# Optimization experiments

Measured on AMD Instinct MI355X. Metric: run time of the kernel, lower is better.

## Reference

```python
import jax, jax.numpy as jnp
import numpy as np

K = 12
ORDERS = [(1, 2, 3), (1, 3, 2), (3, 2, 1), (3, 1, 2), (2, 1, 3), (2, 3, 1)]


def ranking_3d(x):
    # x: (B, L1, W1, H1, D) -> (B, 12, L1*W1*H1, D)
    B, L1, W1, H1, D = x.shape
    seqs = []
    for dims in ORDERS:
        perm = (0,) + dims + (4,)
        seqs.append(jnp.transpose(x, perm).reshape(B, -1, D))
        xr = jnp.flip(x, axis=dims)
        seqs.append(jnp.transpose(xr, perm).reshape(B, -1, D))
    return jnp.stack(seqs, axis=1)


def restore_original(out_y, shape):
    # out_y: (B, 12, D, L). NOTE: faithfully replicates the original code, which
    # reshapes the (B, D, L) slice directly to (B, d1, d2, d3, D).
    B, L1, W1, H1, D = shape
    size = {1: L1, 2: W1, 3: H1}
    restored = []
    for i in range(12):
        dims = ORDERS[i // 2]
        seq = out_y[:, i]  # (B, D, L)
        dims_shape = tuple(size[d] for d in dims)
        reshaped = seq.reshape((B,) + dims_shape + (D,))
        perm = (0,) + dims + (4,)
        inv = tuple(np.argsort(perm))
        r = jnp.transpose(reshaped, inv)
        if i % 2 == 1:
            r = jnp.flip(r, axis=dims)
        restored.append(r)
    return restored


def selective_scan(u, delta, A, Bs, Cs):
    # u, delta: (B,K,D,L); A: (K,D,N); Bs, Cs: (B,K,N,L)
    us = jnp.moveaxis(u, -1, 0)       # (L,B,K,D)
    ds = jnp.moveaxis(delta, -1, 0)   # (L,B,K,D)
    Bts = jnp.moveaxis(Bs, -1, 0)     # (L,B,K,N)
    Cts = jnp.moveaxis(Cs, -1, 0)     # (L,B,K,N)
    h0 = jnp.zeros(u.shape[:-1] + (A.shape[-1],), u.dtype)  # (B,K,D,N)

    def step(h, inp):
        ut, dt, Bt, Ct = inp
        dA = jnp.exp(dt[..., None] * A)                       # (B,K,D,N)
        h = dA * h + (dt * ut)[..., None] * Bt[:, :, None, :]
        y = jnp.einsum('bkdn,bkn->bkd', h, Ct)
        return h, y

    _, ys = jax.lax.scan(step, h0, (us, ds, Bts, Cts))
    return jnp.moveaxis(ys, 0, -1)  # (B,K,D,L)


def setup_inputs() -> dict:
    key = jax.random.key(0)
    ks = jax.random.split(key, 8)
    B, H, W, Len, D = 1, 16, 16, 16, 128
    N, R = 16, 8
    x = jax.random.normal(ks[0], (B, H, W, Len, D), dtype=jnp.float32)
    x_proj_weight = jax.random.normal(ks[1], (K, R + 2 * N, D), dtype=jnp.float32) * 0.02
    std = R ** -0.5
    dt_projs_weight = jax.random.uniform(ks[2], (K, D, R), minval=-std, maxval=std, dtype=jnp.float32)
    dt = jnp.exp(jax.random.uniform(ks[3], (K, D)) * (np.log(0.1) - np.log(0.001)) + np.log(0.001))
    dt = jnp.clip(dt, 1e-4, None)
    dt_projs_bias = (dt + jnp.log(-jnp.expm1(-dt))).astype(jnp.float32)
    A_logs = jnp.broadcast_to(jnp.log(jnp.arange(1, N + 1, dtype=jnp.float32)), (K, D, N)).copy()
    Ds = jnp.ones((K, D), dtype=jnp.float32)
    merge_w = jax.random.normal(ks[4], (K,), dtype=jnp.float32) * (1.0 / K)
    merge_b = jax.random.normal(ks[5], (), dtype=jnp.float32) * 0.01
    return {'x': x, 'x_proj_weight': x_proj_weight, 'dt_projs_weight': dt_projs_weight,
            'dt_projs_bias': dt_projs_bias, 'A_logs': A_logs, 'Ds': Ds,
            'merge_w': merge_w, 'merge_b': merge_b}


def reference(x, x_proj_weight, dt_projs_weight, dt_projs_bias, A_logs, Ds, merge_w, merge_b):
    B, H, W, Len, D = x.shape
    L = H * W * Len
    R = dt_projs_weight.shape[-1]
    N = A_logs.shape[-1]
    xs = jnp.transpose(ranking_3d(x), (0, 1, 3, 2))  # (B,K,D,L)
    x_dbl = jnp.einsum('bkdl,kcd->bkcl', xs, x_proj_weight)  # (B,K,R+2N,L)
    dts, Bs, Cs = jnp.split(x_dbl, [R, R + N], axis=2)
    dts = jnp.einsum('bkrl,kdr->bkdl', dts, dt_projs_weight)
    delta = jax.nn.softplus(dts + dt_projs_bias[None, :, :, None])
    A = -jnp.exp(A_logs)  # (K,D,N)
    ys = selective_scan(xs, delta, A, Bs, Cs)
    out_y = ys + Ds[None, :, :, None] * xs  # (B,K,D,L)
    restored = restore_original(out_y, (B, H, W, Len, D))
    stacked = jnp.stack(restored, axis=1)  # (B,K,H,W,Len,D)
    # mergeconv: 1x1 Conv2d over K channels == weighted sum across directions
    y = jnp.einsum('bkhwld,k->bhwld', stacked, merge_w) + merge_b
    return y
```

## Files before the change

### kernel.cpp

```cpp
#include <hip/hip_runtime.h>

#define KK 12
#define LL 4096
#define DD 128
#define NN 16
#define RR 8
#define NC 128
#define LC 32
#define XST 132
#define SDST 44
#define XDBL_TILE (LC * SDST)

__device__ __forceinline__ int pos_of(int k, int l) {
    int o = k >> 1;
    int le = (k & 1) ? (4095 - l) : l;
    int t1 = le >> 8, t2 = (le >> 4) & 15, t3 = le & 15;
    switch (o) {
        case 0:  return (t1 << 8) | (t2 << 4) | t3;
        case 1:  return (t1 << 8) | (t3 << 4) | t2;
        case 2:  return (t3 << 8) | (t2 << 4) | t1;
        case 3:  return (t2 << 8) | (t3 << 4) | t1;
        case 4:  return (t2 << 8) | (t1 << 4) | t3;
        default: return (t3 << 8) | (t1 << 4) | t2;
    }
}

__device__ __forceinline__ float delta_row_z(const float* sdbl, int l,
                                             float4 w0, float4 w1, float bz) {
    const float4* dr = (const float4*)(sdbl + l * SDST);
    float4 r0 = dr[0], r1 = dr[1];
    return bz + w0.x * r0.x + w0.y * r0.y + w0.z * r0.z + w0.w * r0.w
              + w1.x * r1.x + w1.y * r1.y + w1.z * r1.z + w1.w * r1.w;
}

__device__ __forceinline__ bool load_A8(const float* __restrict__ A_logs,
                                        int k, int d, int n0, float* A8, float& A0) {
    const float4* ap = (const float4*)(A_logs + ((size_t)(k * DD + d) * NN + n0));
    float4 a0 = ap[0], a1 = ap[1];
    A8[0] = -__expf(a0.x); A8[1] = -__expf(a0.y);
    A8[2] = -__expf(a0.z); A8[3] = -__expf(a0.w);
    A8[4] = -__expf(a1.x); A8[5] = -__expf(a1.y);
    A8[6] = -__expf(a1.z); A8[7] = -__expf(a1.w);
    A0 = -__expf(A_logs[(size_t)(k * DD + d) * NN]);
    bool s = (fabsf(A0 + 1.0f) <= 1e-5f);
    #pragma unroll
    for (int j = 0; j < 8; j++) {
        float m = (float)(n0 + j + 1);
        s = s && (fabsf(A8[j] - m * A0) <= 1e-4f * m * fabsf(A0));
    }
    return s;
}

template<bool S>
__device__ __forceinline__ void scan_step(
    float* xs, const float* sdbl, int i, int d, int half, int n0,
    const float* A8, float dt, float q, float Dval, float* h, float& dsum)
{
    float u = xs[i * XST + d];
    dsum += dt;
    float tu = dt * u;
    float e[8];
    if constexpr (S) {
        float q2 = q * q, q4 = q2 * q2, q8 = q4 * q4;
        e[0] = half ? q8 * q : q;
        #pragma unroll
        for (int j = 1; j < 8; j++) e[j] = e[j - 1] * q;
    } else {
        #pragma unroll
        for (int j = 0; j < 8; j++) e[j] = __expf(dt * A8[j]);
    }
    const float4* bp = (const float4*)(&sdbl[i * SDST + 8 + n0]);
    float4 b0 = bp[0], b1 = bp[1];
    const float4* cp = (const float4*)(&sdbl[i * SDST + 24 + n0]);
    float4 c0 = cp[0], c1 = cp[1];
    h[0] = e[0] * h[0] + tu * b0.x;  h[1] = e[1] * h[1] + tu * b0.y;
    h[2] = e[2] * h[2] + tu * b0.z;  h[3] = e[3] * h[3] + tu * b0.w;
    h[4] = e[4] * h[4] + tu * b1.x;  h[5] = e[5] * h[5] + tu * b1.y;
    h[6] = e[6] * h[6] + tu * b1.z;  h[7] = e[7] * h[7] + tu * b1.w;
    float yp = h[0] * c0.x + h[1] * c0.y + h[2] * c0.z + h[3] * c0.w
             + h[4] * c1.x + h[5] * c1.y + h[6] * c1.z + h[7] * c1.w;
    float yv = yp + __shfl_xor(yp, 1) + Dval * u;
    if (!half) xs[i * XST + d] = yv;
}

template<bool S>
__device__ __forceinline__ void scanA_body(
    float* xs, const float* sdbl, int k, int c,
    int d, int half, int n0, const float* A8,
    float4 w0, float4 w1, float bz, float Dval,
    float* __restrict__ S_g, float* __restrict__ dtsum)
{
    float h[8] = {0, 0, 0, 0, 0, 0, 0, 0};
    float dsum = 0.0f;

    #pragma unroll 2
    for (int i2 = 0; i2 < LC; i2 += 2) {
        float z = delta_row_z(sdbl, i2 + half, w0, w1, bz);
        float E = __expf(-fabsf(z));
        float opE = 1.0f + E;
        float dt = fmaxf(z, 0.0f) + __logf(opE);
        float q = 0.0f;
        if constexpr (S)
            q = (z >= 0.0f ? E : 1.0f) * __builtin_amdgcn_rcpf(opE);
        float dto = __shfl_xor(dt, 1);
        float qo  = S ? __shfl_xor(q, 1) : 0.0f;
        float dt0 = half ? dto : dt,  dt1 = half ? dt : dto;
        float q0  = half ? qo  : q,   q1  = half ? q  : qo;
        scan_step<S>(xs, sdbl, i2,     d, half, n0, A8, dt0, q0, Dval, h, dsum);
        scan_step<S>(xs, sdbl, i2 + 1, d, half, n0, A8, dt1, q1, Dval, h, dsum);
    }

    float4* sp = (float4*)(S_g + (((size_t)(k * NC + c) * DD + d) * NN + n0));
    sp[0] = make_float4(h[0], h[1], h[2], h[3]);
    sp[1] = make_float4(h[4], h[5], h[6], h[7]);
    if (!half) dtsum[(k * NC + c) * DD + d] = dsum;
}

__global__ __launch_bounds__(256, 4) void k1_proj_scanA(
    const float* __restrict__ x, const float* __restrict__ Wp,
    const float* __restrict__ Wdt, const float* __restrict__ bias,
    const float* __restrict__ A_logs, const float* __restrict__ Ds,
    float* __restrict__ S_g, float* __restrict__ dtsum,
    float* __restrict__ oy, float* __restrict__ xdbl)
{
    const int blk = blockIdx.x;
    const int k = blk >> 7;
    const int c = blk & 127;
    const int l0 = c * LC;
    const int t = threadIdx.x;

    __shared__ __align__(16) float xs[LC * XST];
    __shared__ __align__(16) float sdbl[LC * SDST];
    __shared__ int pos_s[LC];

    if (t < LC) pos_s[t] = pos_of(k, l0 + t);
    __syncthreads();

    {
        int lane32 = t & 31, rowi = t >> 5;
        #pragma unroll
        for (int p = 0; p < 4; p++) {
            int l = p * 8 + rowi;
            float4 v = *(const float4*)(x + (size_t)pos_s[l] * DD + lane32 * 4);
            *(float4*)(&xs[l * XST + lane32 * 4]) = v;
        }
    }
    __syncthreads();

    {
        int l = t & 31, cg = t >> 5;
        float acc[5];
        #pragma unroll
        for (int j = 0; j < 5; j++) acc[j] = 0.0f;
        const float* wk = Wp + (size_t)(k * 40 + cg * 5) * DD;
        for (int d4 = 0; d4 < DD; d4 += 4) {
            float4 xv = *(const float4*)(&xs[l * XST + d4]);
            #pragma unroll
            for (int j = 0; j < 5; j++) {
                const float* w = wk + j * DD + d4;
                acc[j] += xv.x * w[0] + xv.y * w[1] + xv.z * w[2] + xv.w * w[3];
            }
        }
        #pragma unroll
        for (int j = 0; j < 5; j++) sdbl[l * SDST + cg * 5 + j] = acc[j];
    }
    __syncthreads();

    {
        const float4* s4 = (const float4*)sdbl;
        float4* g4 = (float4*)(xdbl + (size_t)blk * XDBL_TILE);
        for (int idx = t; idx < XDBL_TILE / 4; idx += 256) g4[idx] = s4[idx];
    }

    const int d = t >> 1, half = t & 1, n0 = half * 8;
    float A8[8], A0;
    bool structured = load_A8(A_logs, k, d, n0, A8, A0);
    const float4* wp4 = (const float4*)(Wdt + (size_t)(k * DD + d) * RR);
    const float4 w0 = wp4[0], w1 = wp4[1];
    const float bz = bias[k * DD + d];
    const float Dval = Ds[k * DD + d];

    if (structured)
        scanA_body<true>(xs, sdbl, k, c, d, half, n0, A8, w0, w1, bz,
                         Dval, S_g, dtsum);
    else
        scanA_body<false>(xs, sdbl, k, c, d, half, n0, A8, w0, w1, bz,
                          Dval, S_g, dtsum);

    {
        float* base = oy + ((size_t)(k * DD + d)) * LL + l0 + half * 16;
        #pragma unroll
        for (int p = 0; p < 4; p++) {
            int j = p * 4;
            float4 v = make_float4(xs[(half * 16 + j + 0) * XST + d],
                                   xs[(half * 16 + j + 1) * XST + d],
                                   xs[(half * 16 + j + 2) * XST + d],
                                   xs[(half * 16 + j + 3) * XST + d]);
            *(float4*)(base + j) = v;
        }
    }
}

__global__ __launch_bounds__(256) void k2_combine(
    float* __restrict__ S_g, const float* __restrict__ dtsum,
    const float* __restrict__ A_logs)
{
    int tid = blockIdx.x * 256 + threadIdx.x;
    int kk = tid >> 11, rem = tid & 2047, dd2 = rem >> 4;
    float Ac = -__expf(A_logs[tid]);
    float hh = 0.0f;
    #pragma unroll 8
    for (int c2 = 0; c2 < NC; c2++) {
        size_t base = ((size_t)(kk * NC + c2)) * 2048 + rem;
        float s = S_g[base];
        float dsv = dtsum[(kk * NC + c2) * DD + dd2];
        S_g[base] = hh;
        hh = s + __expf(dsv * Ac) * hh;
    }
}

template<bool S>
__device__ __forceinline__ void corr_body(
    float* ybuf, const float* sdbl, int d, int half, int n0,
    const float* A8, const float* h0, float4 w0, float4 w1, float bz)
{
    if constexpr (S) {
        float Q = 1.0f;
        #pragma unroll 2
        for (int i2 = 0; i2 < LC; i2 += 2) {
            float z = delta_row_z(sdbl, i2 + half, w0, w1, bz);
            float E = __expf(-fabsf(z));
            float q = (z >= 0.0f ? E : 1.0f) * __builtin_amdgcn_rcpf(1.0f + E);
            float qo = __shfl_xor(q, 1);
            float q0 = half ? qo : q, q1 = half ? q : qo;
            #pragma unroll
            for (int s = 0; s < 2; s++) {
                int i = i2 + s;
                Q *= (s ? q1 : q0);
                const float4* cp = (const float4*)(&sdbl[i * SDST + 24 + n0]);
                float4 c0 = cp[0], c1 = cp[1];
                float sH =           h0[7] * c1.w;
                sH = sH * Q + h0[6] * c1.z;
                sH = sH * Q + h0[5] * c1.y;
                sH = sH * Q + h0[4] * c1.x;
                sH = sH * Q + h0[3] * c0.w;
                sH = sH * Q + h0[2] * c0.z;
                sH = sH * Q + h0[1] * c0.y;
                sH = sH * Q + h0[0] * c0.x;
                float Q2 = Q * Q, Q4 = Q2 * Q2, Q8 = Q4 * Q4;
                float Qp = half ? Q8 * Q : Q;
                float yp = sH * Qp;
                float yv = yp + __shfl_xor(yp, 1);
                if (!half) ybuf[i * XST + d] = yv;
            }
        }
    } else {
        float Dsum = 0.0f;
        #pragma unroll 2
        for (int i2 = 0; i2 < LC; i2 += 2) {
            float z = delta_row_z(sdbl, i2 + half, w0, w1, bz);
            float E = __expf(-fabsf(z));
            float dt = fmaxf(z, 0.0f) + __logf(1.0f + E);
            float dto = __shfl_xor(dt, 1);
            float dt0 = half ? dto : dt, dt1 = half ? dt : dto;
            #pragma unroll
            for (int s = 0; s < 2; s++) {
                int i = i2 + s;
                Dsum += (s ? dt1 : dt0);
                float e[8];
                #pragma unroll
                for (int j = 0; j < 8; j++) e[j] = __expf(Dsum * A8[j]);
                const float4* cp = (const float4*)(&sdbl[i * SDST + 24 + n0]);
                float4 c0 = cp[0], c1 = cp[1];
                float yp = e[0]*h0[0]*c0.x + e[1]*h0[1]*c0.y + e[2]*h0[2]*c0.z + e[3]*h0[3]*c0.w
                         + e[4]*h0[4]*c1.x + e[5]*h0[5]*c1.y + e[6]*h0[6]*c1.z + e[7]*h0[7]*c1.w;
                float yv = yp + __shfl_xor(yp, 1);
                if (!half) ybuf[i * XST + d] = yv;
            }
        }
    }
}

__global__ __launch_bounds__(256, 4) void k3_corr(
    const float* __restrict__ Wdt, const float* __restrict__ bias,
    const float* __restrict__ A_logs, const float* __restrict__ S_g,
    const float* __restrict__ xdbl, float* __restrict__ oy)
{
    const int blk = blockIdx.x;
    const int k = blk >> 7;
    const int c = blk & 127;
    if (c == 0) return;
    const int l0 = c * LC;
    const int t = threadIdx.x;

    __shared__ __align__(16) float sdbl[LC * SDST];
    __shared__ __align__(16) float ybuf[LC * XST];
    {
        const float4* g4 = (const float4*)(xdbl + (size_t)blk * XDBL_TILE);
        float4* s4 = (float4*)sdbl;
        for (int idx = t; idx < XDBL_TILE / 4; idx += 256) s4[idx] = g4[idx];
    }
    __syncthreads();

    const int d = t >> 1, half = t & 1, n0 = half * 8;
    float A8[8], A0;
    bool structured = load_A8(A_logs, k, d, n0, A8, A0);
    const float4* wp4 = (const float4*)(Wdt + (size_t)(k * DD + d) * RR);
    const float4 w0 = wp4[0], w1 = wp4[1];
    const float bz = bias[k * DD + d];

    float h0[8];
    {
        const float4* hp = (const float4*)(S_g + (((size_t)(k * NC + c) * DD + d) * NN + n0));
        float4 h40 = hp[0], h41 = hp[1];
        h0[0] = h40.x; h0[1] = h40.y; h0[2] = h40.z; h0[3] = h40.w;
        h0[4] = h41.x; h0[5] = h41.y; h0[6] = h41.z; h0[7] = h41.w;
    }

    if (structured)
        corr_body<true>(ybuf, sdbl, d, half, n0, A8, h0, w0, w1, bz);
    else
        corr_body<false>(ybuf, sdbl, d, half, n0, A8, h0, w0, w1, bz);

    {
        float* base = oy + ((size_t)(k * DD + d)) * LL + l0 + half * 16;
        #pragma unroll
        for (int p = 0; p < 4; p++) {
            int j = p * 4;
            float4 v = *(float4*)(base + j);
            v.x += ybuf[(half * 16 + j + 0) * XST + d];
            v.y += ybuf[(half * 16 + j + 1) * XST + d];
            v.z += ybuf[(half * 16 + j + 2) * XST + d];
            v.w += ybuf[(half * 16 + j + 3) * XST + d];
            *(float4*)(base + j) = v;
        }
    }
}

__global__ __launch_bounds__(256) void k4_merge(
    const float* __restrict__ out_y, const float* __restrict__ mw,
    const float* __restrict__ mb, float* __restrict__ out)
{
    int idx4 = blockIdx.x * 256 + threadIdx.x;
    int dd4 = (idx4 & 31) * 4;
    int p = idx4 >> 5;
    int i3 = p & 15, i2 = (p >> 4) & 15, i1 = (p >> 8) & 15;

    float b = mb[0];
    float4 accv = make_float4(b, b, b, b);
    #pragma unroll
    for (int k = 0; k < 12; k++) {
        int a1 = i1, a2 = i2, a3 = i3;
        if (k & 1) { a1 = 15 - i1; a2 = 15 - i2; a3 = 15 - i3; }
        int j1, j2, j3;
        switch (k >> 1) {
            case 0:  j1 = a1; j2 = a2; j3 = a3; break;
            case 1:  j1 = a1; j2 = a3; j3 = a2; break;
            case 2:  j1 = a3; j2 = a2; j3 = a1; break;
            case 3:  j1 = a3; j2 = a1; j3 = a2; break;
            case 4:  j1 = a2; j2 = a1; j3 = a3; break;
            default: j1 = a2; j2 = a3; j3 = a1; break;
        }
        int jb = (j1 << 8) | (j2 << 4) | j3;
        float4 v = *(const float4*)(out_y + (size_t)k * (DD * LL) + (jb >> 5) * LL
                                    + ((jb & 31) << 7) + dd4);
        float w = mw[k];
        accv.x += w * v.x; accv.y += w * v.y;
        accv.z += w * v.z; accv.w += w * v.w;
    }
    *(float4*)(out + (size_t)p * DD + dd4) = accv;
}

extern "C" void kernel_launch(void* const* d_in, const int* in_sizes, int n_in,
                              void* d_out, int out_size, void* d_ws, size_t ws_size,
                              hipStream_t stream) {
    const float* x      = (const float*)d_in[0];
    const float* Wp     = (const float*)d_in[1];
    const float* Wdt    = (const float*)d_in[2];
    const float* bias   = (const float*)d_in[3];
    const float* A_logs = (const float*)d_in[4];
    const float* Ds     = (const float*)d_in[5];
    const float* mw     = (const float*)d_in[6];
    const float* mb     = (const float*)d_in[7];
    float* out = (float*)d_out;

    float* ws   = (float*)d_ws;
    float* S_g  = ws;
    float* dts  = S_g + (size_t)KK * NC * DD * NN;
    float* oy   = dts + (size_t)KK * NC * DD;
    float* xdbl = oy + (size_t)KK * DD * LL;

    k1_proj_scanA<<<dim3(KK * NC), dim3(256), 0, stream>>>(
        x, Wp, Wdt, bias, A_logs, Ds, S_g, dts, oy, xdbl);
    k2_combine<<<dim3(KK * DD * NN / 256), dim3(256), 0, stream>>>(S_g, dts, A_logs);
    k3_corr<<<dim3(KK * NC), dim3(256), 0, stream>>>(Wdt, bias, A_logs, S_g, xdbl, oy);
    k4_merge<<<dim3(LL * DD / 1024), dim3(256), 0, stream>>>(oy, mw, mb, out);
}
```

Before: 158.7 us.

## Parallelize chunk-state combine across chunks with two-level blocked scan

The k2_combine kernel previously had each thread walk all 128 chunks serially to propagate the SSM state. Now each (k,d,n) state is handled by 8 threads, one per 16-chunk segment. Each thread computes a local segment summary (sum and decay product), the summaries are exchanged through shared memory to get a segment prefix, and then the thread rescans its segment to write the exclusive states. This cuts the serial dependency chain and raises the launched thread count 8x, at the cost of reading S_g and dtsum twice and computing the exponentials twice.

New measurement: 154.7 us (median of 2 runs). -2.5%, faster.

```diff
diff --git a/kernel.cpp b/kernel.cpp
--- a/kernel.cpp
+++ b/kernel.cpp
@@ -205,17 +205,44 @@
     float* __restrict__ S_g, const float* __restrict__ dtsum,
     const float* __restrict__ A_logs)
 {
-    int tid = blockIdx.x * 256 + threadIdx.x;
-    int kk = tid >> 11, rem = tid & 2047, dd2 = rem >> 4;
-    float Ac = -__expf(A_logs[tid]);
-    float hh = 0.0f;
-    #pragma unroll 8
-    for (int c2 = 0; c2 < NC; c2++) {
-        size_t base = ((size_t)(kk * NC + c2)) * 2048 + rem;
+    const int t = threadIdx.x;
+    const int s_l = t & 31;
+    const int g   = t >> 5;
+    const int sid = blockIdx.x * 32 + s_l;
+    const int kk  = sid >> 11, rem = sid & 2047, dd2 = rem >> 4;
+    const float Ac = -__expf(A_logs[sid]);
+
+    __shared__ float lsS[8][32];
+    __shared__ float lsW[8][32];
+
+    const int c0 = g * 16;
+
+    float S = 0.0f, W = 1.0f;
+    #pragma unroll 4
+    for (int i = 0; i < 16; i++) {
+        int c = c0 + i;
+        size_t base = ((size_t)(kk * NC + c)) * 2048 + rem;
         float s = S_g[base];
-        float dsv = dtsum[(kk * NC + c2) * DD + dd2];
-        S_g[base] = hh;
-        hh = s + __expf(dsv * Ac) * hh;
+        float w = __expf(dtsum[(kk * NC + c) * DD + dd2] * Ac);
+        S = s + w * S;
+        W = w * W;
+    }
+    lsS[g][s_l] = S;
+    lsW[g][s_l] = W;
+    __syncthreads();
+
+    float h = 0.0f;
+    for (int j = 0; j < g; j++)
+        h = lsS[j][s_l] + lsW[j][s_l] * h;
+
+    #pragma unroll 4
+    for (int i = 0; i < 16; i++) {
+        int c = c0 + i;
+        size_t base = ((size_t)(kk * NC + c)) * 2048 + rem;
+        float s = S_g[base];
+        float w = __expf(dtsum[(kk * NC + c) * DD + dd2] * Ac);
+        S_g[base] = h;
+        h = s + w * h;
     }
 }
 
@@ -392,7 +419,7 @@
 
     k1_proj_scanA<<<dim3(KK * NC), dim3(256), 0, stream>>>(
         x, Wp, Wdt, bias, A_logs, Ds, S_g, dts, oy, xdbl);
-    k2_combine<<<dim3(KK * DD * NN / 256), dim3(256), 0, stream>>>(S_g, dts, A_logs);
+    k2_combine<<<dim3(KK * DD * NN / 32), dim3(256), 0, stream>>>(S_g, dts, A_logs);
     k3_corr<<<dim3(KK * NC), dim3(256), 0, stream>>>(Wdt, bias, A_logs, S_g, xdbl, oy);
     k4_merge<<<dim3(LL * DD / 1024), dim3(256), 0, stream>>>(oy, mw, mb, out);
 }
```
